# Kernel optimization log

Measured on AMD Instinct MI355X. Metric: run time of the kernel, lower is better.

## Reference

```python
import jax, jax.numpy as jnp
import numpy as np

B, T, E, H, S = 4, 4096, 1024, 16, 64
D = E // H  # head_dim = 64
ROPE_BASE = 10000.0


def _rotate_half(x):
    # interleaved rotate: out[..., 2i] = -x[..., 2i+1]; out[..., 2i+1] = x[..., 2i]
    x1 = x[..., ::2]
    x2 = x[..., 1::2]
    return jnp.stack([-x2, x1], axis=-1).reshape(x.shape)


def _rope_cos_sin(t, d):
    inv_freq = 1.0 / (ROPE_BASE ** (jnp.arange(0, d, 2, dtype=jnp.float32) / d))
    freqs = jnp.arange(t, dtype=jnp.float32)[:, None] * inv_freq[None, :]  # [t, d/2]
    emb = jnp.concatenate([freqs, freqs], axis=-1)  # [t, d]
    # broadcast over batch and heads for q/k of shape [b, t, h, d]
    return jnp.cos(emb)[None, :, None, :], jnp.sin(emb)[None, :, None, :]


def setup_inputs() -> dict:
    key = jax.random.key(0)
    ks = jax.random.split(key, 6)
    s = E ** -0.5
    return {
        "x": jax.random.normal(ks[0], (B, T, E), dtype=jnp.float32),
        "Wq": jax.random.normal(ks[1], (E, E), dtype=jnp.float32) * s,
        "Wk": jax.random.normal(ks[2], (E, E), dtype=jnp.float32) * s,
        "Wv": jax.random.normal(ks[3], (E, E), dtype=jnp.float32) * s,
        "Wout": jax.random.normal(ks[4], (E, E), dtype=jnp.float32) * s,
        "slot_keys": jax.random.normal(ks[5], (H, S, D), dtype=jnp.float32) * (D ** -0.5),
    }


def reference(x, Wq, Wk, Wv, Wout, slot_keys):
    b, t, e = x.shape
    h, s_slots, d = slot_keys.shape
    scale = d ** -0.5

    q = (x @ Wq.T).reshape(b, t, h, d)
    k = (x @ Wk.T).reshape(b, t, h, d)
    v = (x @ Wv.T).reshape(b, t, h, d)

    cos, sin = _rope_cos_sin(t, d)
    q = q * cos + _rotate_half(q) * sin
    k = k * cos + _rotate_half(k) * sin

    # write pass: route each token's value into memory slots
    write_logits = jnp.einsum('bthd,hsd->bths', k, slot_keys) * scale
    write_weights = jax.nn.softmax(write_logits, axis=-1)  # write_temperature = 1.0
    slot_state = jnp.einsum('bths,bthd->bshd', write_weights, v) / t

    # read pass: query the slot memory
    read_logits = jnp.einsum('bthd,bshd->bths', q, slot_state) * scale
    read_weights = jax.nn.softmax(read_logits, axis=-1)  # read_temperature = 1.0
    read_out = jnp.einsum('bths,bshd->bthd', read_weights, slot_state)

    return read_out.reshape(b, t, e) @ Wout.T
```

## Files before the change

kernel.cpp:

```cpp
#include <hip/hip_runtime.h>
#include <cstdint>
#include <cstddef>

#define BB 4
#define TT 4096
#define EE 1024
#define HH 16
#define SSLOTS 64
#define DD 64
#define MM (BB*TT)

typedef unsigned short u16;
typedef __attribute__((ext_vector_type(8))) short s16x8;
typedef __attribute__((ext_vector_type(4))) float f32x4;
typedef __attribute__((ext_vector_type(8))) unsigned short us8v;
typedef __attribute__((ext_vector_type(4))) unsigned short us4v;

#define MFMA16(a, b, c) __builtin_amdgcn_mfma_f32_16x16x32_bf16((a), (b), (c), 0, 0, 0)

__device__ __forceinline__ u16 f2bf(float x) {
  union { float f; uint32_t u; } c; c.f = x;
  uint32_t u = c.u;
  u += 0x7fffu + ((u >> 16) & 1u);
  return (u16)(u >> 16);
}

__device__ __forceinline__ float bf2f(u16 x) {
  union { uint32_t u; float f; } c; c.u = ((uint32_t)x) << 16;
  return c.f;
}

__device__ __forceinline__ void async16(const void* g, void* l) {
  auto lp = reinterpret_cast<__attribute__((address_space(3))) void*>(
      reinterpret_cast<uintptr_t>(l));
  auto gp = reinterpret_cast<const __attribute__((address_space(1))) void*>(
      reinterpret_cast<uintptr_t>(g));
  __builtin_amdgcn_global_load_lds(gp, lp, 16, 0, 0);
}

__device__ __forceinline__ us8v rope8(us8v kv, const float* __restrict__ rcp,
                                      const float* __restrict__ rsp) {
  float e[8];
#pragma unroll
  for (int m = 0; m < 8; ++m) e[m] = bf2f((u16)kv[m]);
  us8v o;
#pragma unroll
  for (int j = 0; j < 4; ++j) {
    float c0 = rcp[2 * j], c1 = rcp[2 * j + 1];
    float s0 = rsp[2 * j], s1 = rsp[2 * j + 1];
    o[2 * j]     = f2bf(e[2 * j] * c0 - e[2 * j + 1] * s0);
    o[2 * j + 1] = f2bf(e[2 * j + 1] * c1 + e[2 * j] * s1);
  }
  return o;
}

__global__ __launch_bounds__(256) void k_prep(const float* __restrict__ x,
                                              const float* __restrict__ w0,
                                              const float* __restrict__ w1,
                                              const float* __restrict__ w2,
                                              const float* __restrict__ w3,
                                              u16* __restrict__ x16,
                                              u16* __restrict__ dW,
                                              u16* __restrict__ dWo,
                                              float* __restrict__ rc,
                                              float* __restrict__ rs) {
  int bid = blockIdx.x;
  if (bid < 16384) {
    int i = (bid * 256 + threadIdx.x) * 4;
    float4 v = *(const float4*)(x + i);
    us4v o = { f2bf(v.x), f2bf(v.y), f2bf(v.z), f2bf(v.w) };
    *(us4v*)(x16 + i) = o;
  } else if (bid < 16384 + 4096) {
    int bb = bid - 16384;
    int sel = bb >> 10;
    const float* s = (sel == 0) ? w0 : (sel == 1) ? w1 : (sel == 2) ? w2 : w3;
    u16* d = (sel < 3) ? (dW + (size_t)sel * EE * EE) : dWo;
    int i = ((bb & 1023) * 256 + threadIdx.x) * 4;
    float4 v = *(const float4*)(s + i);
    us4v o = { f2bf(v.x), f2bf(v.y), f2bf(v.z), f2bf(v.w) };
    *(us4v*)(d + i) = o;
  } else {
    int i = (bid - 16384 - 4096) * 256 + threadIdx.x;
    int t = i >> 5, f = i & 31;
    double invf = pow(10000.0, -(double)(2 * f) / 64.0);
    double th = fmod((double)t * invf, 6.28318530717958647692528676655900577);
    rc[i] = (float)cos(th);
    rs[i] = (float)sin(th);
  }
}

__device__ __forceinline__ void gemm_tile_128(const u16* __restrict__ Ablk,
                                              const u16* __restrict__ Bblk,
                                              int K, u16* As, u16* Bs,
                                              f32x4 acc[4][4]) {
  const int tid = threadIdx.x;
  const int lane = tid & 63, wave = tid >> 6;
  const int l16 = lane & 15, q8 = (lane >> 4) * 8;
  const int wm = (wave >> 1) * 64, wn = (wave & 1) * 64;
  const int ar = tid >> 2, ac = (tid & 3) * 8;
  const u16* Ag0 = Ablk + (size_t)ar * K + ac;
  const u16* Ag1 = Ablk + (size_t)(ar + 64) * K + ac;
  const u16* Bg0 = Bblk + (size_t)ar * K + ac;
  const u16* Bg1 = Bblk + (size_t)(ar + 64) * K + ac;
  u16* Al0 = As + ar * 32 + ac;
  u16* Al1 = As + (ar + 64) * 32 + ac;
  u16* Bl0 = Bs + ar * 32 + ac;
  u16* Bl1 = Bs + (ar + 64) * 32 + ac;

  for (int k0 = 0; k0 < K; k0 += 64) {
    async16(Ag0 + k0, Al0);
    async16(Ag1 + k0, Al1);
    async16(Ag0 + k0 + 32, Al0 + 4096);
    async16(Ag1 + k0 + 32, Al1 + 4096);
    async16(Bg0 + k0, Bl0);
    async16(Bg1 + k0, Bl1);
    async16(Bg0 + k0 + 32, Bl0 + 4096);
    async16(Bg1 + k0 + 32, Bl1 + 4096);
    __syncthreads();
#pragma unroll
    for (int p = 0; p < 2; ++p) {
      const u16* Ap = As + p * 4096;
      const u16* Bp = Bs + p * 4096;
      s16x8 af[4], bf[4];
#pragma unroll
      for (int i = 0; i < 4; ++i) {
        af[i] = *(const s16x8*)(Ap + (wm + i * 16 + l16) * 32 + q8);
        bf[i] = *(const s16x8*)(Bp + (wn + i * 16 + l16) * 32 + q8);
      }
#pragma unroll
      for (int im = 0; im < 4; ++im)
#pragma unroll
        for (int in = 0; in < 4; ++in)
          acc[im][in] = MFMA16(af[im], bf[in], acc[im][in]);
    }
    __syncthreads();
  }
}

__global__ __launch_bounds__(256) void k_gemm_qkv(const u16* __restrict__ A,
                                                  const u16* __restrict__ Bw,
                                                  u16* __restrict__ q16,
                                                  u16* __restrict__ k16,
                                                  u16* __restrict__ v16) {
  __shared__ u16 As[2 * 128 * 32];
  __shared__ u16 Bs[2 * 128 * 32];
  f32x4 acc[4][4];
#pragma unroll
  for (int i = 0; i < 4; ++i)
#pragma unroll
    for (int j = 0; j < 4; ++j) acc[i][j] = (f32x4){0.f, 0.f, 0.f, 0.f};

  const int m0 = blockIdx.x * 128;
  const int n0g = blockIdx.y * 128;
  gemm_tile_128(A + (size_t)m0 * 1024, Bw + (size_t)n0g * 1024, 1024, As, Bs, acc);

  const int tid = threadIdx.x, lane = tid & 63, wave = tid >> 6;
  const int l16 = lane & 15, q4 = lane >> 4;
  const int wm = (wave >> 1) * 64, wn = (wave & 1) * 64;
  const int which = n0g >> 10;
  const int nb = n0g & 1023;
  u16* dst = (which == 0) ? q16 : ((which == 1) ? k16 : v16);

#pragma unroll
  for (int im = 0; im < 4; ++im)
#pragma unroll
    for (int in = 0; in < 4; ++in)
#pragma unroll
      for (int reg = 0; reg < 4; ++reg) {
        float v = acc[im][in][reg];
        int m = m0 + wm + im * 16 + q4 * 4 + reg;
        int nn = nb + wn + in * 16 + l16;
        int b = m >> 12, t = m & 4095;
        int h = nn >> 6, d = nn & 63;
        dst[((size_t)(b * HH + h) * TT + t) * 64 + d] = f2bf(v);
      }
}

__global__ __launch_bounds__(256) void k_gemm_out(const u16* __restrict__ A,
                                                  const u16* __restrict__ Bw,
                                                  float* __restrict__ C) {
  __shared__ u16 As[2 * 128 * 32];
  __shared__ u16 Bs[2 * 128 * 32];
  f32x4 acc[4][4];
#pragma unroll
  for (int i = 0; i < 4; ++i)
#pragma unroll
    for (int j = 0; j < 4; ++j) acc[i][j] = (f32x4){0.f, 0.f, 0.f, 0.f};

  const int m0 = blockIdx.x * 128;
  const int n0 = blockIdx.y * 128;
  gemm_tile_128(A + (size_t)m0 * 1024, Bw + (size_t)n0 * 1024, 1024, As, Bs, acc);

  const int tid = threadIdx.x, lane = tid & 63, wave = tid >> 6;
  const int l16 = lane & 15, q4 = lane >> 4;
  const int wm = (wave >> 1) * 64, wn = (wave & 1) * 64;
#pragma unroll
  for (int im = 0; im < 4; ++im)
#pragma unroll
    for (int in = 0; in < 4; ++in)
#pragma unroll
      for (int reg = 0; reg < 4; ++reg) {
        int m = m0 + wm + im * 16 + q4 * 4 + reg;
        int n = n0 + wn + in * 16 + l16;
        C[(size_t)m * 1024 + n] = acc[im][in][reg];
      }
}

__global__ __launch_bounds__(256) void k_stage2(const u16* __restrict__ K16g,
                                                const u16* __restrict__ V16g,
                                                const float* __restrict__ SKg,
                                                const float* __restrict__ rc,
                                                const float* __restrict__ rs,
                                                float* __restrict__ SSb) {
  const int tid = threadIdx.x, lane = tid & 63, wave = tid >> 6;
  const int l16 = lane & 15, q4 = lane >> 4, q8 = q4 * 8;
  const int bh = blockIdx.x >> 3, cb = blockIdx.x & 7;
  const int h = bh & 15;

  __shared__ u16 Ks[128 * 88];
  __shared__ u16 Vs[64 * 136];
  __shared__ u16 SKs[64 * 88];
  u16* ww = Ks;

  const float* skh = SKg + (size_t)h * (SSLOTS * DD);
  for (int i = tid; i < 4096; i += 256)
    SKs[(i >> 6) * 88 + (i & 63)] = f2bf(skh[i]);

  f32x4 a2[4];
#pragma unroll
  for (int in = 0; in < 4; ++in) a2[in] = (f32x4){0.f, 0.f, 0.f, 0.f};

  const int w32 = wave * 32;
  for (int cc = 0; cc < 4; ++cc) {
    const int tg0 = cb * 512 + cc * 128;
    __syncthreads();

    const u16* ks = K16g + ((size_t)bh * TT + tg0) * 64;
    for (int idx = tid; idx < 1024; idx += 256) {
      int t = idx >> 3, p = idx & 7;
      us8v kv = *(const us8v*)(ks + (size_t)t * 64 + p * 8);
      int fi = (tg0 + t) * 32 + ((p * 8) & 31);
      us8v kr = rope8(kv, rc + fi, rs + fi);
      *(us8v*)&Ks[t * 88 + p * 8] = kr;
    }
    const u16* vsrc = V16g + ((size_t)bh * TT + tg0) * 64;
    for (int idx = tid; idx < 1024; idx += 256) {
      int t = idx & 127, dg = idx >> 7;
      us8v vv = *(const us8v*)(vsrc + (size_t)t * 64 + dg * 8);
#pragma unroll
      for (int j = 0; j < 8; ++j) Vs[(dg * 8 + j) * 136 + t] = vv[j];
    }
    __syncthreads();

    f32x4 a1[2][4];
#pragma unroll
    for (int im = 0; im < 2; ++im)
#pragma unroll
      for (int in = 0; in < 4; ++in) a1[im][in] = (f32x4){0.f, 0.f, 0.f, 0.f};
#pragma unroll
    for (int ksx = 0; ksx < 2; ++ksx) {
      s16x8 afr0 = *(const s16x8*)&Ks[(w32 + l16) * 88 + ksx * 32 + q8];
      s16x8 afr1 = *(const s16x8*)&Ks[(w32 + 16 + l16) * 88 + ksx * 32 + q8];
#pragma unroll
      for (int in = 0; in < 4; ++in) {
        s16x8 bfr = *(const s16x8*)&SKs[(in * 16 + l16) * 88 + ksx * 32 + q8];
        a1[0][in] = MFMA16(afr0, bfr, a1[0][in]);
        a1[1][in] = MFMA16(afr1, bfr, a1[1][in]);
      }
    }
    __syncthreads();

#pragma unroll
    for (int im = 0; im < 2; ++im)
#pragma unroll
      for (int reg = 0; reg < 4; ++reg) {
        float v0 = a1[im][0][reg] * 0.125f, v1 = a1[im][1][reg] * 0.125f;
        float v2 = a1[im][2][reg] * 0.125f, v3 = a1[im][3][reg] * 0.125f;
        float mx = fmaxf(fmaxf(v0, v1), fmaxf(v2, v3));
#pragma unroll
        for (int m = 1; m < 16; m <<= 1) mx = fmaxf(mx, __shfl_xor(mx, m));
        float e0 = __expf(v0 - mx), e1 = __expf(v1 - mx);
        float e2 = __expf(v2 - mx), e3 = __expf(v3 - mx);
        float sm = e0 + e1 + e2 + e3;
#pragma unroll
        for (int m = 1; m < 16; m <<= 1) sm += __shfl_xor(sm, m);
        float inv = 1.0f / sm;
        int tl = w32 + im * 16 + q4 * 4 + reg;
        ww[(l16) * 136 + tl]      = f2bf(e0 * inv);
        ww[(16 + l16) * 136 + tl] = f2bf(e1 * inv);
        ww[(32 + l16) * 136 + tl] = f2bf(e2 * inv);
        ww[(48 + l16) * 136 + tl] = f2bf(e3 * inv);
      }
    __syncthreads();

#pragma unroll
    for (int ksx = 0; ksx < 4; ++ksx) {
      s16x8 afr = *(const s16x8*)&ww[(wave * 16 + l16) * 136 + ksx * 32 + q8];
#pragma unroll
      for (int in = 0; in < 4; ++in) {
        s16x8 bfr = *(const s16x8*)&Vs[(in * 16 + l16) * 136 + ksx * 32 + q8];
        a2[in] = MFMA16(afr, bfr, a2[in]);
      }
    }
  }

  const float invT = 1.0f / (float)TT;
#pragma unroll
  for (int in = 0; in < 4; ++in)
#pragma unroll
    for (int reg = 0; reg < 4; ++reg) {
      int s = wave * 16 + q4 * 4 + reg;
      int d = in * 16 + l16;
      atomicAdd(&SSb[(size_t)bh * 4096 + s * 64 + d], a2[in][reg] * invT);
    }
}

__global__ __launch_bounds__(256) void k_stage3(const u16* __restrict__ Q16g,
                                                const float* __restrict__ SSg,
                                                const float* __restrict__ rc,
                                                const float* __restrict__ rs,
                                                u16* __restrict__ RO) {
  const int tid = threadIdx.x, lane = tid & 63, wave = tid >> 6;
  const int l16 = lane & 15, q4 = lane >> 4, q8 = q4 * 8;
  const int bh = blockIdx.x >> 5, ck = blockIdx.x & 31;
  const int b = bh >> 4, h = bh & 15;
  const int tg0 = ck * 128;

  __shared__ u16 Qs[128 * 88];
  __shared__ u16 ss_sd[64 * 88];
  __shared__ u16 ss_ds[64 * 88];
  u16* RWs = Qs;

  const float* ssp = SSg + (size_t)bh * 4096;
  for (int i = tid; i < 4096; i += 256) {
    u16 u = f2bf(ssp[i]);
    int s = i >> 6, d = i & 63;
    ss_sd[s * 88 + d] = u;
    ss_ds[d * 88 + s] = u;
  }
  const u16* qsrc = Q16g + ((size_t)bh * TT + tg0) * 64;
  for (int idx = tid; idx < 1024; idx += 256) {
    int t = idx >> 3, p = idx & 7;
    us8v qv = *(const us8v*)(qsrc + (size_t)t * 64 + p * 8);
    int fi = (tg0 + t) * 32 + ((p * 8) & 31);
    us8v qr = rope8(qv, rc + fi, rs + fi);
    *(us8v*)&Qs[t * 88 + p * 8] = qr;
  }
  __syncthreads();

  const int w32 = wave * 32;
  f32x4 a3[2][4];
#pragma unroll
  for (int i = 0; i < 2; ++i)
#pragma unroll
    for (int j = 0; j < 4; ++j) a3[i][j] = (f32x4){0.f, 0.f, 0.f, 0.f};
#pragma unroll
  for (int ksx = 0; ksx < 2; ++ksx) {
    s16x8 afr[2];
#pragma unroll
    for (int im = 0; im < 2; ++im)
      afr[im] = *(const s16x8*)&Qs[(w32 + im * 16 + l16) * 88 + ksx * 32 + q8];
#pragma unroll
    for (int in = 0; in < 4; ++in) {
      s16x8 bfr = *(const s16x8*)&ss_sd[(in * 16 + l16) * 88 + ksx * 32 + q8];
#pragma unroll
      for (int im = 0; im < 2; ++im) a3[im][in] = MFMA16(afr[im], bfr, a3[im][in]);
    }
  }
  __syncthreads();

#pragma unroll
  for (int im = 0; im < 2; ++im)
#pragma unroll
    for (int reg = 0; reg < 4; ++reg) {
      float v0 = a3[im][0][reg] * 0.125f, v1 = a3[im][1][reg] * 0.125f;
      float v2 = a3[im][2][reg] * 0.125f, v3 = a3[im][3][reg] * 0.125f;
      float mx = fmaxf(fmaxf(v0, v1), fmaxf(v2, v3));
#pragma unroll
      for (int m = 1; m < 16; m <<= 1) mx = fmaxf(mx, __shfl_xor(mx, m));
      float e0 = __expf(v0 - mx), e1 = __expf(v1 - mx);
      float e2 = __expf(v2 - mx), e3 = __expf(v3 - mx);
      float sm = e0 + e1 + e2 + e3;
#pragma unroll
      for (int m = 1; m < 16; m <<= 1) sm += __shfl_xor(sm, m);
      float inv = 1.0f / sm;
      int tl = w32 + im * 16 + q4 * 4 + reg;
      RWs[tl * 88 + l16]      = f2bf(e0 * inv);
      RWs[tl * 88 + 16 + l16] = f2bf(e1 * inv);
      RWs[tl * 88 + 32 + l16] = f2bf(e2 * inv);
      RWs[tl * 88 + 48 + l16] = f2bf(e3 * inv);
    }
  __syncthreads();

  f32x4 a4[2][4];
#pragma unroll
  for (int i = 0; i < 2; ++i)
#pragma unroll
    for (int j = 0; j < 4; ++j) a4[i][j] = (f32x4){0.f, 0.f, 0.f, 0.f};
#pragma unroll
  for (int ksx = 0; ksx < 2; ++ksx) {
    s16x8 afr[2];
#pragma unroll
    for (int im = 0; im < 2; ++im)
      afr[im] = *(const s16x8*)&RWs[(w32 + im * 16 + l16) * 88 + ksx * 32 + q8];
#pragma unroll
    for (int in = 0; in < 4; ++in) {
      s16x8 bfr = *(const s16x8*)&ss_ds[(in * 16 + l16) * 88 + ksx * 32 + q8];
#pragma unroll
      for (int im = 0; im < 2; ++im) a4[im][in] = MFMA16(afr[im], bfr, a4[im][in]);
    }
  }

#pragma unroll
  for (int im = 0; im < 2; ++im)
#pragma unroll
    for (int in = 0; in < 4; ++in)
#pragma unroll
      for (int reg = 0; reg < 4; ++reg) {
        int t = tg0 + w32 + im * 16 + q4 * 4 + reg;
        int d = in * 16 + l16;
        RO[((size_t)b * TT + t) * 1024 + h * 64 + d] = f2bf(a4[im][in][reg]);
      }
}

extern "C" void kernel_launch(void* const* d_in, const int* in_sizes, int n_in,
                              void* d_out, int out_size, void* d_ws, size_t ws_size,
                              hipStream_t stream) {
  const float* x  = (const float*)d_in[0];
  const float* Wq = (const float*)d_in[1];
  const float* Wk = (const float*)d_in[2];
  const float* Wv = (const float*)d_in[3];
  const float* Wo = (const float*)d_in[4];
  const float* SK = (const float*)d_in[5];
  float* out = (float*)d_out;

  char* w = (char*)d_ws;
  u16* x16 = (u16*)w;   w += (size_t)MM * EE * 2;
  u16* W16 = (u16*)w;   w += (size_t)3 * EE * EE * 2;
  u16* Wo16 = (u16*)w;  w += (size_t)EE * EE * 2;
  u16* Q16 = (u16*)w;   w += (size_t)BB * HH * TT * DD * 2;
  u16* K16 = (u16*)w;   w += (size_t)BB * HH * TT * DD * 2;
  u16* V16 = (u16*)w;   w += (size_t)BB * HH * TT * DD * 2;
  float* SSb = (float*)w; w += (size_t)BB * HH * SSLOTS * DD * 4;
  float* rc = (float*)w;  w += (size_t)TT * 32 * 4;
  float* rs = (float*)w;  w += (size_t)TT * 32 * 4;
  u16* RO16 = x16;

  if ((size_t)(w - (char*)d_ws) > ws_size) return;

  k_prep<<<16384 + 4096 + 512, 256, 0, stream>>>(x, Wq, Wk, Wv, Wo, x16, W16, Wo16, rc, rs);

  k_gemm_qkv<<<dim3(MM / 128, 3 * EE / 128), 256, 0, stream>>>(x16, W16, Q16, K16, V16);

  hipMemsetAsync(SSb, 0, (size_t)BB * HH * SSLOTS * DD * 4, stream);
  k_stage2<<<512, 256, 0, stream>>>(K16, V16, SK, rc, rs, SSb);
  k_stage3<<<2048, 256, 0, stream>>>(Q16, SSb, rc, rs, RO16);

  k_gemm_out<<<dim3(MM / 128, EE / 128), 256, 0, stream>>>(RO16, Wo16, out);
}
```

Before: 347.8 us.

## Replace 128x128 GEMMs with 256x256 swizzled, pipelined 8-wave MFMA GEMM

Replaces the 128x128 bf16 GEMM tile used by the QKV and output projections with a 256x256 tile run by 512 threads. It uses XOR-swizzled LDS layouts to avoid bank conflicts, a double-buffered async load pipeline with split-phase barriers, s_setprio around the MFMA bursts, and a block-index swizzle for L2 locality. The goal is more data reuse per tile and global-load latency hidden behind MFMA work. In exchange it uses 128KB of LDS per block and far more accumulator registers, which limits occupancy, and the output GEMM launches only 256 blocks.

Result: no change. 342.3 us (-1.6%).

```diff
diff --git a/kernel.cpp b/kernel.cpp
--- a/kernel.cpp
+++ b/kernel.cpp
@@ -89,118 +89,193 @@
   }
 }
 
-__device__ __forceinline__ void gemm_tile_128(const u16* __restrict__ Ablk,
-                                              const u16* __restrict__ Bblk,
-                                              int K, u16* As, u16* Bs,
-                                              f32x4 acc[4][4]) {
-  const int tid = threadIdx.x;
-  const int lane = tid & 63, wave = tid >> 6;
-  const int l16 = lane & 15, q8 = (lane >> 4) * 8;
-  const int wm = (wave >> 1) * 64, wn = (wave & 1) * 64;
-  const int ar = tid >> 2, ac = (tid & 3) * 8;
-  const u16* Ag0 = Ablk + (size_t)ar * K + ac;
-  const u16* Ag1 = Ablk + (size_t)(ar + 64) * K + ac;
-  const u16* Bg0 = Bblk + (size_t)ar * K + ac;
-  const u16* Bg1 = Bblk + (size_t)(ar + 64) * K + ac;
-  u16* Al0 = As + ar * 32 + ac;
-  u16* Al1 = As + (ar + 64) * 32 + ac;
-  u16* Bl0 = Bs + ar * 32 + ac;
-  u16* Bl1 = Bs + (ar + 64) * 32 + ac;
-
-  for (int k0 = 0; k0 < K; k0 += 64) {
-    async16(Ag0 + k0, Al0);
-    async16(Ag1 + k0, Al1);
-    async16(Ag0 + k0 + 32, Al0 + 4096);
-    async16(Ag1 + k0 + 32, Al1 + 4096);
-    async16(Bg0 + k0, Bl0);
-    async16(Bg1 + k0, Bl1);
-    async16(Bg0 + k0 + 32, Bl0 + 4096);
-    async16(Bg1 + k0 + 32, Bl1 + 4096);
-    __syncthreads();
-#pragma unroll
-    for (int p = 0; p < 2; ++p) {
-      const u16* Ap = As + p * 4096;
-      const u16* Bp = Bs + p * 4096;
-      s16x8 af[4], bf[4];
-#pragma unroll
-      for (int i = 0; i < 4; ++i) {
-        af[i] = *(const s16x8*)(Ap + (wm + i * 16 + l16) * 32 + q8);
-        bf[i] = *(const s16x8*)(Bp + (wn + i * 16 + l16) * 32 + q8);
-      }
-#pragma unroll
-      for (int im = 0; im < 4; ++im)
-#pragma unroll
-        for (int in = 0; in < 4; ++in)
-          acc[im][in] = MFMA16(af[im], bf[in], acc[im][in]);
-    }
-    __syncthreads();
-  }
-}
-
-__global__ __launch_bounds__(256) void k_gemm_qkv(const u16* __restrict__ A,
-                                                  const u16* __restrict__ Bw,
-                                                  u16* __restrict__ q16,
-                                                  u16* __restrict__ k16,
-                                                  u16* __restrict__ v16) {
-  __shared__ u16 As[2 * 128 * 32];
-  __shared__ u16 Bs[2 * 128 * 32];
-  f32x4 acc[4][4];
-#pragma unroll
-  for (int i = 0; i < 4; ++i)
-#pragma unroll
-    for (int j = 0; j < 4; ++j) acc[i][j] = (f32x4){0.f, 0.f, 0.f, 0.f};
-
-  const int m0 = blockIdx.x * 128;
-  const int n0g = blockIdx.y * 128;
-  gemm_tile_128(A + (size_t)m0 * 1024, Bw + (size_t)n0g * 1024, 1024, As, Bs, acc);
-
+
+__device__ __forceinline__ void mm16(f32x4 (&acc)[8][4], const s16x8* a,
+                                     const s16x8* b, int ab) {
+#pragma unroll
+  for (int im = 0; im < 4; ++im)
+#pragma unroll
+    for (int in = 0; in < 4; ++in)
+      acc[ab + im][in] = MFMA16(a[im], b[in], acc[ab + im][in]);
+}
+
+__device__ __forceinline__ void gemm256(const u16* __restrict__ A,
+                                        const u16* __restrict__ B,
+                                        char* smem, f32x4 (&acc)[8][4]) {
   const int tid = threadIdx.x, lane = tid & 63, wave = tid >> 6;
   const int l16 = lane & 15, q4 = lane >> 4;
-  const int wm = (wave >> 1) * 64, wn = (wave & 1) * 64;
-  const int which = n0g >> 10;
-  const int nb = n0g & 1023;
+  const int wrow = (wave >> 2) * 128;
+  const int wcol = (wave & 3) * 64;
+
+  const int sr0 = wave * 32 + (lane >> 2);
+  const int sr1 = sr0 + 16;
+  const int sc  = (lane & 3) * 16;
+  const size_t ga0 = (size_t)sr0 * 2048 + (size_t)(sc ^ (((sr0 >> 1) & 3) << 4));
+  const size_t ga1 = (size_t)sr1 * 2048 + (size_t)(sc ^ (((sr1 >> 1) & 3) << 4));
+  const int lo0 = sr0 * 64 + sc;
+  const int lo1 = sr1 * 64 + sc;
+  const char* Ab = (const char*)A;
+  const char* Bb = (const char*)B;
+
+  int offA[8], offB[4];
+#pragma unroll
+  for (int f = 0; f < 8; ++f) {
+    int r = wrow + f * 16 + l16;
+    offA[f] = (r * 64 + q4 * 16) ^ (((r >> 1) & 3) << 4);
+  }
+#pragma unroll
+  for (int f = 0; f < 4; ++f) {
+    int r = wcol + f * 16 + l16;
+    offB[f] = (r * 64 + q4 * 16) ^ (((r >> 1) & 3) << 4);
+  }
+
+#define STG(dst, srcb, kb) do { \
+    async16((srcb) + (size_t)(kb) + ga0, (dst) + lo0); \
+    async16((srcb) + (size_t)(kb) + ga1, (dst) + lo1); } while (0)
+
+  STG(smem +     0, Ab, 0);
+  STG(smem + 32768, Bb, 0);
+  STG(smem + 16384, Ab, 64);
+  STG(smem + 49152, Bb, 64);
+  STG(smem + 65536 +     0, Ab, 128);
+  STG(smem + 65536 + 32768, Bb, 128);
+  asm volatile("s_waitcnt vmcnt(4)" ::: "memory");
+  __builtin_amdgcn_s_barrier();
+
+  for (int tau = 0; tau < 16; ++tau) {
+    char* cb = smem + ((tau & 1) << 16);
+    char* nb = smem + (((tau + 1) & 1) << 16);
+    const char* Ak0 = cb;
+    const char* Ak1 = cb + 16384;
+    const char* Bk0 = cb + 32768;
+    const char* Bk1 = cb + 49152;
+    const int kb1 = (tau + 1) << 7;
+    const int kb2 = (tau + 2) << 7;
+    const bool st1 = tau < 15, st2 = tau < 14;
+
+    s16x8 a[4], b[4];
+
+#pragma unroll
+    for (int f = 0; f < 4; ++f) a[f] = *(const s16x8*)(Ak0 + offA[f]);
+#pragma unroll
+    for (int f = 0; f < 4; ++f) b[f] = *(const s16x8*)(Bk0 + offB[f]);
+    if (st1) STG(nb + 16384, Ab, kb1 + 64);
+    __builtin_amdgcn_s_barrier();
+    asm volatile("s_waitcnt lgkmcnt(0)" ::: "memory");
+    __builtin_amdgcn_sched_barrier(0);
+    __builtin_amdgcn_s_setprio(1);
+    mm16(acc, a, b, 0);
+    __builtin_amdgcn_s_setprio(0);
+    __builtin_amdgcn_s_barrier();
+
+#pragma unroll
+    for (int f = 0; f < 4; ++f) a[f] = *(const s16x8*)(Ak0 + offA[4 + f]);
+    if (st1) STG(nb + 49152, Bb, kb1 + 64);
+    __builtin_amdgcn_s_barrier();
+    asm volatile("s_waitcnt lgkmcnt(0)" ::: "memory");
+    __builtin_amdgcn_sched_barrier(0);
+    __builtin_amdgcn_s_setprio(1);
+    mm16(acc, a, b, 4);
+    __builtin_amdgcn_s_setprio(0);
+    __builtin_amdgcn_s_barrier();
+
+#pragma unroll
+    for (int f = 0; f < 4; ++f) a[f] = *(const s16x8*)(Ak1 + offA[f]);
+#pragma unroll
+    for (int f = 0; f < 4; ++f) b[f] = *(const s16x8*)(Bk1 + offB[f]);
+    if (st2) STG(cb, Ab, kb2);
+    __builtin_amdgcn_s_barrier();
+    asm volatile("s_waitcnt lgkmcnt(0)" ::: "memory");
+    __builtin_amdgcn_sched_barrier(0);
+    __builtin_amdgcn_s_setprio(1);
+    mm16(acc, a, b, 0);
+    __builtin_amdgcn_s_setprio(0);
+    __builtin_amdgcn_s_barrier();
+
+#pragma unroll
+    for (int f = 0; f < 4; ++f) a[f] = *(const s16x8*)(Ak1 + offA[4 + f]);
+    if (st2) STG(cb + 32768, Bb, kb2);
+    if (tau < 14) asm volatile("s_waitcnt vmcnt(4)" ::: "memory");
+    else          asm volatile("s_waitcnt vmcnt(0)" ::: "memory");
+    __builtin_amdgcn_s_barrier();
+    asm volatile("s_waitcnt lgkmcnt(0)" ::: "memory");
+    __builtin_amdgcn_sched_barrier(0);
+    __builtin_amdgcn_s_setprio(1);
+    mm16(acc, a, b, 4);
+    __builtin_amdgcn_s_setprio(0);
+    __builtin_amdgcn_s_barrier();
+  }
+#undef STG
+}
+
+__global__ __launch_bounds__(512, 2) void k_gemm_qkv(const u16* __restrict__ A,
+                                                     const u16* __restrict__ Bw,
+                                                     u16* __restrict__ q16,
+                                                     u16* __restrict__ k16,
+                                                     u16* __restrict__ v16) {
+  __shared__ char smem[131072];
+  const int bid = blockIdx.x;
+  const int swz = (bid & 7) * 96 + (bid >> 3);
+  const int mt = swz & 63, nt = swz >> 6;
+  const int m0 = mt * 256, n0 = nt * 256;
+
+  f32x4 acc[8][4];
+#pragma unroll
+  for (int i = 0; i < 8; ++i)
+#pragma unroll
+    for (int j = 0; j < 4; ++j) acc[i][j] = (f32x4){0.f, 0.f, 0.f, 0.f};
+
+  gemm256(A + (size_t)m0 * 1024, Bw + (size_t)n0 * 1024, smem, acc);
+
+  const int tid = threadIdx.x, lane = tid & 63, wave = tid >> 6;
+  const int l16 = lane & 15, q4 = lane >> 4;
+  const int wrow = (wave >> 2) * 128, wn = (wave & 3) * 64;
+  const int which = n0 >> 10;
+  const int nbl = n0 & 1023;
   u16* dst = (which == 0) ? q16 : ((which == 1) ? k16 : v16);
 
 #pragma unroll
-  for (int im = 0; im < 4; ++im)
+  for (int im = 0; im < 8; ++im)
 #pragma unroll
     for (int in = 0; in < 4; ++in)
 #pragma unroll
       for (int reg = 0; reg < 4; ++reg) {
         float v = acc[im][in][reg];
-        int m = m0 + wm + im * 16 + q4 * 4 + reg;
-        int nn = nb + wn + in * 16 + l16;
-        int b = m >> 12, t = m & 4095;
+        int m = m0 + wrow + im * 16 + q4 * 4 + reg;
+        int nn = nbl + wn + in * 16 + l16;
+        int bq = m >> 12, t = m & 4095;
         int h = nn >> 6, d = nn & 63;
-        dst[((size_t)(b * HH + h) * TT + t) * 64 + d] = f2bf(v);
+        dst[((size_t)(bq * HH + h) * TT + t) * 64 + d] = f2bf(v);
       }
 }
 
-__global__ __launch_bounds__(256) void k_gemm_out(const u16* __restrict__ A,
-                                                  const u16* __restrict__ Bw,
-                                                  float* __restrict__ C) {
-  __shared__ u16 As[2 * 128 * 32];
-  __shared__ u16 Bs[2 * 128 * 32];
-  f32x4 acc[4][4];
-#pragma unroll
-  for (int i = 0; i < 4; ++i)
+__global__ __launch_bounds__(512, 2) void k_gemm_out(const u16* __restrict__ A,
+                                                     const u16* __restrict__ Bw,
+                                                     float* __restrict__ C) {
+  __shared__ char smem[131072];
+  const int bid = blockIdx.x;
+  const int swz = (bid & 7) * 32 + (bid >> 3);
+  const int mt = swz & 63, nt = swz >> 6;
+  const int m0 = mt * 256, n0 = nt * 256;
+
+  f32x4 acc[8][4];
+#pragma unroll
+  for (int i = 0; i < 8; ++i)
 #pragma unroll
     for (int j = 0; j < 4; ++j) acc[i][j] = (f32x4){0.f, 0.f, 0.f, 0.f};
 
-  const int m0 = blockIdx.x * 128;
-  const int n0 = blockIdx.y * 128;
-  gemm_tile_128(A + (size_t)m0 * 1024, Bw + (size_t)n0 * 1024, 1024, As, Bs, acc);
+  gemm256(A + (size_t)m0 * 1024, Bw + (size_t)n0 * 1024, smem, acc);
 
   const int tid = threadIdx.x, lane = tid & 63, wave = tid >> 6;
   const int l16 = lane & 15, q4 = lane >> 4;
-  const int wm = (wave >> 1) * 64, wn = (wave & 1) * 64;
-#pragma unroll
-  for (int im = 0; im < 4; ++im)
+  const int wrow = (wave >> 2) * 128, wn = (wave & 3) * 64;
+#pragma unroll
+  for (int im = 0; im < 8; ++im)
 #pragma unroll
     for (int in = 0; in < 4; ++in)
 #pragma unroll
       for (int reg = 0; reg < 4; ++reg) {
-        int m = m0 + wm + im * 16 + q4 * 4 + reg;
+        int m = m0 + wrow + im * 16 + q4 * 4 + reg;
         int n = n0 + wn + in * 16 + l16;
         C[(size_t)m * 1024 + n] = acc[im][in][reg];
       }
@@ -450,11 +525,11 @@
 
   k_prep<<<16384 + 4096 + 512, 256, 0, stream>>>(x, Wq, Wk, Wv, Wo, x16, W16, Wo16, rc, rs);
 
-  k_gemm_qkv<<<dim3(MM / 128, 3 * EE / 128), 256, 0, stream>>>(x16, W16, Q16, K16, V16);
+  k_gemm_qkv<<<768, 512, 0, stream>>>(x16, W16, Q16, K16, V16);
 
   hipMemsetAsync(SSb, 0, (size_t)BB * HH * SSLOTS * DD * 4, stream);
   k_stage2<<<512, 256, 0, stream>>>(K16, V16, SK, rc, rs, SSb);
   k_stage3<<<2048, 256, 0, stream>>>(Q16, SSb, rc, rs, RO16);
 
-  k_gemm_out<<<dim3(MM / 128, EE / 128), 256, 0, stream>>>(RO16, Wo16, out);
-}
+  k_gemm_out<<<256, 512, 0, stream>>>(RO16, Wo16, out);
+}
```
